# Performance work log

Measured on AMD Instinct MI355X. Metric: run time of the kernel, lower is better.

Reference implementation:

```python
import jax, jax.numpy as jnp
import numpy as np

C = 512
H = 8
P = 64
B = 4
N = 1024


def setup_inputs() -> dict:
    key = jax.random.key(0)
    ks = jax.random.split(key, 12)
    s = 0.02
    return {
        "tokens": jax.random.normal(ks[0], (B, N, C), dtype=jnp.float32),
        "pair_features": jax.random.normal(ks[1], (N, N, P), dtype=jnp.float32),
        "Wq": jax.random.normal(ks[2], (C, C), dtype=jnp.float32) * s,
        "bq": jnp.zeros((C,), dtype=jnp.float32),
        "Wk": jax.random.normal(ks[3], (C, C), dtype=jnp.float32) * s,
        "bk": jnp.zeros((C,), dtype=jnp.float32),
        "Wv": jax.random.normal(ks[4], (C, C), dtype=jnp.float32) * s,
        "bv": jnp.zeros((C,), dtype=jnp.float32),
        "Wo": jax.random.normal(ks[5], (C, C), dtype=jnp.float32) * s,
        "bo": jnp.zeros((C,), dtype=jnp.float32),
        "Wp": jax.random.normal(ks[6], (P, H), dtype=jnp.float32) * s,
    }


def reference(tokens, pair_features, Wq, bq, Wk, bk, Wv, bv, Wo, bo, Wp):
    b, n, c = tokens.shape
    h = H
    d = c // h
    scale = d ** -0.5
    # projections -> [b, h, n, d]
    q = (tokens @ Wq + bq).reshape(b, n, h, d).transpose(0, 2, 1, 3)
    k = (tokens @ Wk + bk).reshape(b, n, h, d).transpose(0, 2, 1, 3)
    v = (tokens @ Wv + bv).reshape(b, n, h, d).transpose(0, 2, 1, 3)
    # attention logits [b, h, n, n] with additive pair-derived bias [h, n, n]
    logits = jnp.einsum('bhnd,bhmd->bhnm', q, k) * scale
    pair_bias = jnp.einsum('nmp,ph->hnm', pair_features, Wp)
    logits = logits + pair_bias[None]
    attn = jax.nn.softmax(logits, axis=-1)  # dropout p=0.0 -> identity
    merged = jnp.einsum('bhnm,bhmd->bhnd', attn, v)
    merged = merged.transpose(0, 2, 1, 3).reshape(b, n, c)
    return merged @ Wo + bo
```

## Files before the change

### kernel.cpp

```cpp
#include <hip/hip_runtime.h>
#include <hip/hip_bf16.h>
#include <stdint.h>
#include <stddef.h>

typedef __bf16 bf16x8 __attribute__((ext_vector_type(8)));
typedef __bf16 bf16x4 __attribute__((ext_vector_type(4)));
typedef float  f32x4  __attribute__((ext_vector_type(4)));
typedef uint32_t __attribute__((address_space(3))) lds_u32;
typedef uint32_t __attribute__((address_space(1))) glob_u32;

#define QKV_BLOCKS 384
#define PAIR_BLOCKS 2048
#define NSPLIT 2
#define NITER  8
#define LOG2E 1.4426950408889634f

__global__ __launch_bounds__(256) void k1_kernel(
    const float* __restrict__ tokens, const float* __restrict__ pf,
    const float* __restrict__ Wq, const float* __restrict__ Wk,
    const float* __restrict__ Wv, const float* __restrict__ Wp,
    const float* __restrict__ bq, const float* __restrict__ bk,
    const float* __restrict__ bv,
    __bf16* __restrict__ qb, __bf16* __restrict__ kb, __bf16* __restrict__ vtb,
    __bf16* __restrict__ pbb) {
  __shared__ __align__(16) char smem_raw[37504];
  int bx = blockIdx.x, tid = threadIdx.x;
  if (bx < QKV_BLOCKS) {
    __bf16 (*As)[40] = (__bf16(*)[40])smem_raw;
    __bf16 (*Bs)[40] = (__bf16(*)[40])(smem_raw + 10240);
    float (*ftile)[133] = (float(*)[133])(smem_raw + 20480);
    const float qscale = 0.125f * LOG2E;
    int nb = bx % 12, mb = bx / 12;
    int m0 = mb * 128, n0 = nb * 128;
    int sel = n0 >> 9, cloc = n0 & 511;
    const float* W = sel == 0 ? Wq : sel == 1 ? Wk : Wv;
    int wave = tid >> 6, lane = tid & 63;
    int wm = (wave >> 1) * 64, wn = (wave & 1) * 64;
    int lg = lane >> 4, lr = lane & 15;
    f32x4 acc[4][4];
#pragma unroll
    for (int i = 0; i < 4; ++i)
#pragma unroll
      for (int j = 0; j < 4; ++j) acc[i][j] = (f32x4){0.f, 0.f, 0.f, 0.f};

    for (int k0 = 0; k0 < 512; k0 += 32) {
      __syncthreads();
#pragma unroll
      for (int i = 0; i < 2; ++i) {
        int cid = tid + i * 256;
        int row = cid >> 2, c8 = (cid & 3) * 8;
        const float* src = &tokens[(size_t)(m0 + row) * 512 + k0 + c8];
        f32x4 f0 = *(const f32x4*)src, f1 = *(const f32x4*)(src + 4);
        bf16x8 vv;
#pragma unroll
        for (int u = 0; u < 4; ++u) { vv[u] = (__bf16)f0[u]; vv[u + 4] = (__bf16)f1[u]; }
        *(bf16x8*)&As[row][c8] = vv;
      }
#pragma unroll
      for (int i = 0; i < 2; ++i) {
        int cid = tid + i * 256;
        int kk = cid >> 4, n8 = (cid & 15) * 8;
        const float* src = &W[(size_t)(k0 + kk) * 512 + cloc + n8];
        *(f32x4*)&ftile[kk][n8] = *(const f32x4*)src;
        *(f32x4*)&ftile[kk][n8 + 4] = *(const f32x4*)(src + 4);
      }
      __syncthreads();
#pragma unroll
      for (int i = 0; i < 2; ++i) {
        int cid = tid + i * 256;
        int n = cid >> 2, kk8 = (cid & 3) * 8;
        bf16x8 vv;
#pragma unroll
        for (int u = 0; u < 8; ++u) vv[u] = (__bf16)ftile[kk8 + u][n];
        *(bf16x8*)&Bs[n][kk8] = vv;
      }
      __syncthreads();
      bf16x8 af[4], bfr[4];
#pragma unroll
      for (int i = 0; i < 4; ++i) {
        af[i]  = *(const bf16x8*)&As[wm + i * 16 + lr][lg * 8];
        bfr[i] = *(const bf16x8*)&Bs[wn + i * 16 + lr][lg * 8];
      }
#pragma unroll
      for (int i = 0; i < 4; ++i)
#pragma unroll
        for (int j = 0; j < 4; ++j)
          acc[i][j] = __builtin_amdgcn_mfma_f32_16x16x32_bf16(af[i], bfr[j], acc[i][j], 0, 0, 0);
    }
#pragma unroll
    for (int i = 0; i < 4; ++i)
#pragma unroll
      for (int j = 0; j < 4; ++j) {
        int grow0 = m0 + wm + i * 16 + lg * 4;
        int gcol = n0 + wn + j * 16 + lr;
        int gsel = gcol >> 9, c = gcol & 511;
        int hh = c >> 6, dd = c & 63;
        int b = grow0 >> 10, n = grow0 & 1023;
        if (gsel == 2) {
          float bias = bv[c];
          bf16x4 pack;
#pragma unroll
          for (int r = 0; r < 4; ++r) pack[r] = (__bf16)(acc[i][j][r] + bias);
          *(bf16x4*)&vtb[(((size_t)(b * 8 + hh)) * 64 + dd) * 1024 + n] = pack;
        } else if (gsel == 0) {
          float bias = bq[c];
#pragma unroll
          for (int r = 0; r < 4; ++r)
            qb[(((size_t)(b * 8 + hh)) * 1024 + n + r) * 64 + dd] = (__bf16)((acc[i][j][r] + bias) * qscale);
        } else {
          float bias = bk[c];
#pragma unroll
          for (int r = 0; r < 4; ++r)
            kb[(((size_t)(b * 8 + hh)) * 1024 + n + r) * 64 + dd] = (__bf16)(acc[i][j][r] + bias);
        }
      }
  } else {
    int pb = bx - QKV_BLOCKS;
    int wave = tid >> 6, lane = tid & 63;
    int lg = lane >> 4, lr = lane & 15;
    bf16x8 wfrag[2];
#pragma unroll
    for (int s = 0; s < 2; ++s)
#pragma unroll
      for (int j = 0; j < 8; ++j) {
        int p = s * 32 + lg * 8 + j;
        wfrag[s][j] = (lr < 8) ? (__bf16)Wp[p * 8 + lr] : (__bf16)0.f;
      }
    char* psbase = smem_raw + wave * 4096;
    int wbase = pb * 512 + wave * 128;
    int wrow_lo = lane >> 4;
    int wcol = lane & 15;

    f32x4 v[4][4];
    auto PLOAD = [&](int it, int slot) {
      const float* base = pf + (size_t)(wbase + it * 16) * 64;
#pragma unroll
      for (int j = 0; j < 4; ++j)
        v[slot][j] = *(const f32x4*)(base + j * 256 + lane * 4);
    };
    auto PWLDS = [&](int it, int slot) {
      char* ps = psbase + (it & 1) * 2048;
#pragma unroll
      for (int j = 0; j < 4; ++j) {
        int jr = j * 4 + wrow_lo;
        bf16x4 b;
#pragma unroll
        for (int u = 0; u < 4; ++u) b[u] = (__bf16)v[slot][j][u];
        int cbyte = ((((wcol >> 1) ^ (jr & 7)) << 4) | ((wcol & 1) << 3));
        *(bf16x4*)(ps + jr * 128 + cbyte) = b;
      }
    };
    auto PCOMP = [&](int it) {
      char* ps = psbase + (it & 1) * 2048;
      bf16x8 af[2];
#pragma unroll
      for (int s = 0; s < 2; ++s) {
        int cb = ((s * 4 + lg) ^ (lr & 7)) << 4;
        af[s] = *(const bf16x8*)(ps + lr * 128 + cb);
      }
      f32x4 acc = {0.f, 0.f, 0.f, 0.f};
      acc = __builtin_amdgcn_mfma_f32_16x16x32_bf16(af[0], wfrag[0], acc, 0, 0, 0);
      acc = __builtin_amdgcn_mfma_f32_16x16x32_bf16(af[1], wfrag[1], acc, 0, 0, 0);
      if (lr < 8) {
        bf16x4 pk;
#pragma unroll
        for (int r = 0; r < 4; ++r) pk[r] = (__bf16)(acc[r] * LOG2E);
        *(bf16x4*)&pbb[((size_t)lr << 20) + wbase + it * 16 + lg * 4] = pk;
      }
    };

    PLOAD(0, 0);
    PLOAD(1, 1);
    PLOAD(2, 2);
#pragma unroll
    for (int it = 0; it < 8; ++it) {
      if (it + 3 < 8) PLOAD(it + 3, (it + 3) & 3);
      PWLDS(it, it & 3);
      PCOMP(it);
    }
  }
}

__device__ __forceinline__ bf16x8 swz_read(const __bf16* buf, int r, int k) {
  int chunk = (r << 3) | (k ^ (r & 7));
  return *(const bf16x8*)&buf[chunk * 8];
}

__global__ __launch_bounds__(256) void flash_kernel(const __bf16* __restrict__ qg,
                                                    const __bf16* __restrict__ kg,
                                                    const __bf16* __restrict__ vtg,
                                                    const __bf16* __restrict__ pbg,
                                                    float* __restrict__ po,
                                                    float2* __restrict__ ml) {
  __shared__ __align__(16) __bf16 kvs[2][2][64 * 64];
  __shared__ __bf16 pls[4][16][72];
  int bh = blockIdx.y, z = blockIdx.z, h = bh & 7;
  int q0 = blockIdx.x * 64;
  int tid = threadIdx.x, wave = tid >> 6, lane = tid & 63;
  int lg = lane >> 4, lr = lane & 15;
  const __bf16* qp = qg + (size_t)bh * 65536;
  const __bf16* kp = kg + (size_t)bh * 65536;
  const __bf16* vp = vtg + (size_t)bh * 65536;
  const __bf16* pbh = pbg + ((size_t)h << 20);
  int qw0 = q0 + wave * 16;
  int kb0 = z * NITER;

  auto stage = [&](int buf, int kb2) {
#pragma unroll
    for (int p = 0; p < 2; ++p) {
      int c = p * 256 + wave * 64 + lane;
      int r = c >> 3, kk = c & 7;
      int g = (c & ~7) | (kk ^ (r & 7));
      const __bf16* gk = kp + (size_t)kb2 * 4096 + g * 8;
      const __bf16* gv = vp + (size_t)(g >> 3) * 1024 + kb2 * 64 + (g & 7) * 8;
      __builtin_amdgcn_global_load_lds((const glob_u32*)gk,
          (lds_u32*)&kvs[buf][0][(size_t)(p * 256 + wave * 64) * 8], 16, 0, 0);
      __builtin_amdgcn_global_load_lds((const glob_u32*)gv,
          (lds_u32*)&kvs[buf][1][(size_t)(p * 256 + wave * 64) * 8], 16, 0, 0);
    }
  };

  bf16x8 qf[2];
#pragma unroll
  for (int c = 0; c < 2; ++c)
    qf[c] = *(const bf16x8*)&qp[(size_t)(qw0 + lr) * 64 + c * 32 + lg * 8];

  float mrow = -1e30f, lrow = 0.f;
  f32x4 of[4] = {};

  stage(0, kb0);
  __syncthreads();

#pragma unroll
  for (int t = 0; t < NITER; ++t) {
    int kb2 = kb0 + t;
    if (t + 1 < NITER) stage((t + 1) & 1, kb2 + 1);
    const __bf16* kbuf = &kvs[t & 1][0][0];
    const __bf16* vbuf = &kvs[t & 1][1][0];

    bf16x8 kf[4][2];
#pragma unroll
    for (int n = 0; n < 4; ++n)
#pragma unroll
      for (int c = 0; c < 2; ++c)
        kf[n][c] = swz_read(kbuf, n * 16 + lr, c * 4 + lg);

    f32x4 sv[4];
#pragma unroll
    for (int n = 0; n < 4; ++n) {
      bf16x4 bias = *(const bf16x4*)&pbh[(size_t)(qw0 + lr) * 1024 + kb2 * 64 + n * 16 + lg * 4];
      f32x4 cb;
#pragma unroll
      for (int r = 0; r < 4; ++r) cb[r] = (float)bias[r];
      cb = __builtin_amdgcn_mfma_f32_16x16x32_bf16(kf[n][0], qf[0], cb, 0, 0, 0);
      cb = __builtin_amdgcn_mfma_f32_16x16x32_bf16(kf[n][1], qf[1], cb, 0, 0, 0);
      sv[n] = cb;
    }

    float tm = -1e30f;
#pragma unroll
    for (int n = 0; n < 4; ++n)
#pragma unroll
      for (int r = 0; r < 4; ++r) tm = fmaxf(tm, sv[n][r]);
    tm = fmaxf(tm, __shfl_xor(tm, 16));
    tm = fmaxf(tm, __shfl_xor(tm, 32));
    float newm = fmaxf(mrow, tm);
    float fs = exp2f(mrow - newm);
    mrow = newm;
    float rs = 0.f;
#pragma unroll
    for (int n = 0; n < 4; ++n)
#pragma unroll
      for (int r = 0; r < 4; ++r) {
        float p = exp2f(sv[n][r] - newm);
        sv[n][r] = p;
        rs += p;
      }
    rs += __shfl_xor(rs, 16);
    rs += __shfl_xor(rs, 32);
    lrow = lrow * fs + rs;

#pragma unroll
    for (int n = 0; n < 4; ++n) {
      bf16x4 pk;
#pragma unroll
      for (int r = 0; r < 4; ++r) pk[r] = (__bf16)sv[n][r];
      *(bf16x4*)&pls[wave][lr][n * 16 + lg * 4] = pk;
    }

#pragma unroll
    for (int r = 0; r < 4; ++r) {
      float fsq = __shfl(fs, (lane & 48) | (lg * 4 + r));
#pragma unroll
      for (int dn = 0; dn < 4; ++dn) of[dn][r] *= fsq;
    }

    bf16x8 pa[2];
#pragma unroll
    for (int c = 0; c < 2; ++c)
      pa[c] = *(const bf16x8*)&pls[wave][lr][c * 32 + lg * 8];
    bf16x8 vf[4][2];
#pragma unroll
    for (int dn = 0; dn < 4; ++dn)
#pragma unroll
      for (int c = 0; c < 2; ++c)
        vf[dn][c] = swz_read(vbuf, dn * 16 + lr, c * 4 + lg);
#pragma unroll
    for (int dn = 0; dn < 4; ++dn) {
      of[dn] = __builtin_amdgcn_mfma_f32_16x16x32_bf16(pa[0], vf[dn][0], of[dn], 0, 0, 0);
      of[dn] = __builtin_amdgcn_mfma_f32_16x16x32_bf16(pa[1], vf[dn][1], of[dn], 0, 0, 0);
    }
    __syncthreads();
  }

  if (lg == 0)
    ml[(size_t)z * 32768 + bh * 1024 + qw0 + lr] = make_float2(mrow, lrow);
#pragma unroll
  for (int r = 0; r < 4; ++r) {
    int q = qw0 + lg * 4 + r;
#pragma unroll
    for (int dn = 0; dn < 4; ++dn)
      po[((size_t)z * 32768 + bh * 1024 + q) * 64 + dn * 16 + lr] = of[dn][r];
  }
}

__global__ __launch_bounds__(256) void out_gemm_kernel(const float* __restrict__ po,
                                                       const float2* __restrict__ ml,
                                                       const float* __restrict__ Wo,
                                                       const float* __restrict__ bo,
                                                       float* __restrict__ out) {
  __shared__ __bf16 As[128][40];
  __shared__ __bf16 Bs[128][40];
  __shared__ float ftile[32][133];
  int m0 = blockIdx.y * 128, n0 = blockIdx.x * 128;
  int tid = threadIdx.x, wave = tid >> 6, lane = tid & 63;
  int wm = (wave >> 1) * 64, wn = (wave & 1) * 64, lg = lane >> 4, lr = lane & 15;
  f32x4 acc[4][4];
#pragma unroll
  for (int i = 0; i < 4; ++i)
#pragma unroll
    for (int j = 0; j < 4; ++j) acc[i][j] = (f32x4){0.f, 0.f, 0.f, 0.f};

  for (int k0 = 0; k0 < 512; k0 += 32) {
    __syncthreads();
    int h = k0 >> 6;
    int dbase = k0 & 63;
#pragma unroll
    for (int i = 0; i < 2; ++i) {
      int cid = tid + i * 256;
      int row = cid >> 2, c8 = (cid & 3) * 8;
      int grow = m0 + row;
      int b = grow >> 10, q = grow & 1023;
      int rowg = (b * 8 + h) * 1024 + q;
      float2 s0 = ml[rowg], s1 = ml[32768 + rowg];
      float M = fmaxf(s0.x, s1.x);
      float w0 = exp2f(s0.x - M), w1 = exp2f(s1.x - M);
      float inv = 1.f / (w0 * s0.y + w1 * s1.y);
      const float* p0 = &po[(size_t)rowg * 64 + dbase + c8];
      const float* p1 = &po[(size_t)(32768 + rowg) * 64 + dbase + c8];
      bf16x8 vv;
#pragma unroll
      for (int u = 0; u < 8; ++u)
        vv[u] = (__bf16)((w0 * p0[u] + w1 * p1[u]) * inv);
      *(bf16x8*)&As[row][c8] = vv;
    }
#pragma unroll
    for (int i = 0; i < 2; ++i) {
      int cid = tid + i * 256;
      int kk = cid >> 4, n8 = (cid & 15) * 8;
      const float* src = &Wo[(size_t)(k0 + kk) * 512 + n0 + n8];
      *(f32x4*)&ftile[kk][n8] = *(const f32x4*)src;
      *(f32x4*)&ftile[kk][n8 + 4] = *(const f32x4*)(src + 4);
    }
    __syncthreads();
#pragma unroll
    for (int i = 0; i < 2; ++i) {
      int cid = tid + i * 256;
      int n = cid >> 2, kk8 = (cid & 3) * 8;
      bf16x8 v;
#pragma unroll
      for (int u = 0; u < 8; ++u) v[u] = (__bf16)ftile[kk8 + u][n];
      *(bf16x8*)&Bs[n][kk8] = v;
    }
    __syncthreads();
    bf16x8 af[4], bfr[4];
#pragma unroll
    for (int i = 0; i < 4; ++i) {
      af[i]  = *(const bf16x8*)&As[wm + i * 16 + lr][lg * 8];
      bfr[i] = *(const bf16x8*)&Bs[wn + i * 16 + lr][lg * 8];
    }
#pragma unroll
    for (int i = 0; i < 4; ++i)
#pragma unroll
      for (int j = 0; j < 4; ++j)
        acc[i][j] = __builtin_amdgcn_mfma_f32_16x16x32_bf16(af[i], bfr[j], acc[i][j], 0, 0, 0);
  }
#pragma unroll
  for (int i = 0; i < 4; ++i)
#pragma unroll
    for (int j = 0; j < 4; ++j)
#pragma unroll
      for (int r = 0; r < 4; ++r) {
        int grow = m0 + wm + i * 16 + lg * 4 + r;
        int gcol = n0 + wn + j * 16 + lr;
        out[(size_t)grow * 512 + gcol] = acc[i][j][r] + bo[gcol];
      }
}

extern "C" void kernel_launch(void* const* d_in, const int* in_sizes, int n_in,
                              void* d_out, int out_size, void* d_ws, size_t ws_size,
                              hipStream_t stream) {
  const float* tokens = (const float*)d_in[0];
  const float* pf     = (const float*)d_in[1];
  const float* Wq     = (const float*)d_in[2];
  const float* bq     = (const float*)d_in[3];
  const float* Wk     = (const float*)d_in[4];
  const float* bk     = (const float*)d_in[5];
  const float* Wv     = (const float*)d_in[6];
  const float* bv     = (const float*)d_in[7];
  const float* Wo     = (const float*)d_in[8];
  const float* bo     = (const float*)d_in[9];
  const float* Wp     = (const float*)d_in[10];
  float* out = (float*)d_out;

  char* ws = (char*)d_ws;
  size_t off = 0;
  auto alloc = [&](size_t bytes) { char* p = ws + off; off += (bytes + 255) & ~(size_t)255; return p; };
  __bf16* qb     = (__bf16*)alloc((size_t)32 * 1024 * 64 * 2);
  __bf16* kb     = (__bf16*)alloc((size_t)32 * 1024 * 64 * 2);
  __bf16* vtb    = (__bf16*)alloc((size_t)32 * 64 * 1024 * 2);
  __bf16* pbb    = (__bf16*)alloc((size_t)8 * 1024 * 1024 * 2);
  float*  po     = (float*)alloc((size_t)NSPLIT * 32 * 1024 * 64 * 4);
  float2* ml     = (float2*)alloc((size_t)NSPLIT * 32 * 1024 * 8);

  k1_kernel<<<QKV_BLOCKS + PAIR_BLOCKS, 256, 0, stream>>>(
      tokens, pf, Wq, Wk, Wv, Wp, bq, bk, bv, qb, kb, vtb, pbb);
  flash_kernel<<<dim3(16, 32, NSPLIT), 256, 0, stream>>>(qb, kb, vtb, pbb, po, ml);
  out_gemm_kernel<<<dim3(4, 32), 256, 0, stream>>>(po, ml, Wo, bo, out);
}
```

Before: 132.8 us.

## Remove flash split-KV and write normalized bf16 merged output directly

Flash attention now processes the full key range in one block instead of two splits, normalizes by the row sum in the epilogue, and writes bf16 merged activations in [b,n,c] layout. The output GEMM then loads bf16 tiles directly instead of combining two fp32 partials with max/sum rescaling. This removes a large fp32 intermediate round-trip and the merge arithmetic. In exchange, the flash grid is halved, which lowers parallelism and latency hiding.

```diff
diff --git a/kernel.cpp b/kernel.cpp
--- a/kernel.cpp
+++ b/kernel.cpp
@@ -11,8 +11,7 @@
 
 #define QKV_BLOCKS 384
 #define PAIR_BLOCKS 2048
-#define NSPLIT 2
-#define NITER  8
+#define NITER  16
 #define LOG2E 1.4426950408889634f
 
 __global__ __launch_bounds__(256) void k1_kernel(
@@ -190,11 +189,10 @@
                                                     const __bf16* __restrict__ kg,
                                                     const __bf16* __restrict__ vtg,
                                                     const __bf16* __restrict__ pbg,
-                                                    float* __restrict__ po,
-                                                    float2* __restrict__ ml) {
+                                                    __bf16* __restrict__ merged) {
   __shared__ __align__(16) __bf16 kvs[2][2][64 * 64];
   __shared__ __bf16 pls[4][16][72];
-  int bh = blockIdx.y, z = blockIdx.z, h = bh & 7;
+  int bh = blockIdx.y, b = bh >> 3, h = bh & 7;
   int q0 = blockIdx.x * 64;
   int tid = threadIdx.x, wave = tid >> 6, lane = tid & 63;
   int lg = lane >> 4, lr = lane & 15;
@@ -203,7 +201,6 @@
   const __bf16* vp = vtg + (size_t)bh * 65536;
   const __bf16* pbh = pbg + ((size_t)h << 20);
   int qw0 = q0 + wave * 16;
-  int kb0 = z * NITER;
 
   auto stage = [&](int buf, int kb2) {
 #pragma unroll
@@ -228,13 +225,12 @@
   float mrow = -1e30f, lrow = 0.f;
   f32x4 of[4] = {};
 
-  stage(0, kb0);
+  stage(0, 0);
   __syncthreads();
 
 #pragma unroll
   for (int t = 0; t < NITER; ++t) {
-    int kb2 = kb0 + t;
-    if (t + 1 < NITER) stage((t + 1) & 1, kb2 + 1);
+    if (t + 1 < NITER) stage((t + 1) & 1, t + 1);
     const __bf16* kbuf = &kvs[t & 1][0][0];
     const __bf16* vbuf = &kvs[t & 1][1][0];
 
@@ -248,7 +244,7 @@
     f32x4 sv[4];
 #pragma unroll
     for (int n = 0; n < 4; ++n) {
-      bf16x4 bias = *(const bf16x4*)&pbh[(size_t)(qw0 + lr) * 1024 + kb2 * 64 + n * 16 + lg * 4];
+      bf16x4 bias = *(const bf16x4*)&pbh[(size_t)(qw0 + lr) * 1024 + t * 64 + n * 16 + lg * 4];
       f32x4 cb;
 #pragma unroll
       for (int r = 0; r < 4; ++r) cb[r] = (float)bias[r];
@@ -313,19 +309,19 @@
     __syncthreads();
   }
 
-  if (lg == 0)
-    ml[(size_t)z * 32768 + bh * 1024 + qw0 + lr] = make_float2(mrow, lrow);
 #pragma unroll
   for (int r = 0; r < 4; ++r) {
+    float linv = 1.f / __shfl(lrow, (lane & 48) | (lg * 4 + r));
     int q = qw0 + lg * 4 + r;
 #pragma unroll
-    for (int dn = 0; dn < 4; ++dn)
-      po[((size_t)z * 32768 + bh * 1024 + q) * 64 + dn * 16 + lr] = of[dn][r];
+    for (int dn = 0; dn < 4; ++dn) {
+      int dd = dn * 16 + lr;
+      merged[((size_t)(b * 1024 + q)) * 512 + h * 64 + dd] = (__bf16)(of[dn][r] * linv);
+    }
   }
 }
 
-__global__ __launch_bounds__(256) void out_gemm_kernel(const float* __restrict__ po,
-                                                       const float2* __restrict__ ml,
+__global__ __launch_bounds__(256) void out_gemm_kernel(const __bf16* __restrict__ A,
                                                        const float* __restrict__ Wo,
                                                        const float* __restrict__ bo,
                                                        float* __restrict__ out) {
@@ -343,26 +339,11 @@
 
   for (int k0 = 0; k0 < 512; k0 += 32) {
     __syncthreads();
-    int h = k0 >> 6;
-    int dbase = k0 & 63;
 #pragma unroll
     for (int i = 0; i < 2; ++i) {
       int cid = tid + i * 256;
       int row = cid >> 2, c8 = (cid & 3) * 8;
-      int grow = m0 + row;
-      int b = grow >> 10, q = grow & 1023;
-      int rowg = (b * 8 + h) * 1024 + q;
-      float2 s0 = ml[rowg], s1 = ml[32768 + rowg];
-      float M = fmaxf(s0.x, s1.x);
-      float w0 = exp2f(s0.x - M), w1 = exp2f(s1.x - M);
-      float inv = 1.f / (w0 * s0.y + w1 * s1.y);
-      const float* p0 = &po[(size_t)rowg * 64 + dbase + c8];
-      const float* p1 = &po[(size_t)(32768 + rowg) * 64 + dbase + c8];
-      bf16x8 vv;
-#pragma unroll
-      for (int u = 0; u < 8; ++u)
-        vv[u] = (__bf16)((w0 * p0[u] + w1 * p1[u]) * inv);
-      *(bf16x8*)&As[row][c8] = vv;
+      *(bf16x8*)&As[row][c8] = *(const bf16x8*)&A[(size_t)(m0 + row) * 512 + k0 + c8];
     }
 #pragma unroll
     for (int i = 0; i < 2; ++i) {
@@ -430,11 +411,10 @@
   __bf16* kb     = (__bf16*)alloc((size_t)32 * 1024 * 64 * 2);
   __bf16* vtb    = (__bf16*)alloc((size_t)32 * 64 * 1024 * 2);
   __bf16* pbb    = (__bf16*)alloc((size_t)8 * 1024 * 1024 * 2);
-  float*  po     = (float*)alloc((size_t)NSPLIT * 32 * 1024 * 64 * 4);
-  float2* ml     = (float2*)alloc((size_t)NSPLIT * 32 * 1024 * 8);
+  __bf16* merged = (__bf16*)alloc((size_t)4096 * 512 * 2);
 
   k1_kernel<<<QKV_BLOCKS + PAIR_BLOCKS, 256, 0, stream>>>(
       tokens, pf, Wq, Wk, Wv, Wp, bq, bk, bv, qb, kb, vtb, pbb);
-  flash_kernel<<<dim3(16, 32, NSPLIT), 256, 0, stream>>>(qb, kb, vtb, pbb, po, ml);
-  out_gemm_kernel<<<dim3(4, 32), 256, 0, stream>>>(po, ml, Wo, bo, out);
+  flash_kernel<<<dim3(16, 32), 256, 0, stream>>>(qb, kb, vtb, pbb, merged);
+  out_gemm_kernel<<<dim3(4, 32), 256, 0, stream>>>(merged, Wo, bo, out);
 }
```

New measurement: 119.9 us, median of 2. -9.7%, faster.
